# Kernel tuning notes

Hardware: AMD Instinct MI355X
Metric: run time of the kernel (lower is better)

The kernel has to match this reference:

```python
import jax, jax.numpy as jnp
import numpy as np

M, K, N = 8192, 4096, 4096

def setup_inputs() -> dict:
    key = jax.random.key(0)
    k1, k2 = jax.random.split(key)
    x_q = jax.random.randint(k1, (M, K), -128, 128, dtype=jnp.int8)
    weight_q = jax.random.randint(k2, (N, K), -128, 128, dtype=jnp.int8)
    scale_x = jnp.float32(0.02)
    weight_scale = jnp.float32(1.0)
    out_scale = jnp.float32(1.0)
    return {"x_q": x_q, "scale_x": scale_x, "weight_q": weight_q,
            "weight_scale": weight_scale, "out_scale": out_scale}

def reference(x_q, scale_x, weight_q, weight_scale, out_scale):
    # int8 GEMM with int32 accumulation: [M,K] @ [K,N] -> [M,N] int32
    acc = jnp.matmul(x_q.astype(jnp.int32), weight_q.T.astype(jnp.int32))
    # fused dequant + requant scale, then round/clamp back to int8
    scale = scale_x * weight_scale / out_scale
    y = acc.astype(jnp.float32) * scale
    y_q = jnp.clip(jnp.round(y), -128, 127).astype(jnp.int8)
    return (y_q, out_scale)
```

## Files before the change

kernel.cpp:

```cpp
#include <hip/hip_runtime.h>
#include <stdint.h>

#define M_DIM 8192
#define K_DIM 4096
#define N_DIM 4096
#define BM 128
#define BN 128
#define BK 64

typedef __attribute__((ext_vector_type(4))) int i32x4;

__global__ __launch_bounds__(256) void pack_kernel(const int* __restrict__ src,
                                                   int8_t* __restrict__ dst,
                                                   int n4) {
  const int stride = gridDim.x * 256;
  for (int i = blockIdx.x * 256 + threadIdx.x; i < n4; i += stride) {
    int4 v = reinterpret_cast<const int4*>(src)[i];
    int p = (v.x & 0xff) | ((v.y & 0xff) << 8) |
            ((v.z & 0xff) << 16) | ((v.w & 0xff) << 24);
    reinterpret_cast<int*>(dst)[i] = p;
  }
}

__global__ void tail_kernel(float* __restrict__ out, const float* __restrict__ so) {
  out[(size_t)M_DIM * N_DIM] = so[0];
}

template <bool DIRECT>
__global__ __launch_bounds__(256) void gemm_kernel(
    const int8_t* __restrict__ A8, const int8_t* __restrict__ B8,
    const int* __restrict__ A32, const int* __restrict__ B32,
    float* __restrict__ out,
    const float* __restrict__ sx, const float* __restrict__ sw,
    const float* __restrict__ so) {
  __shared__ int8_t As[BM * BK];
  __shared__ int8_t Bs[BN * BK];

  const int tid = threadIdx.x;
  const int lane = tid & 63;
  const int wid = tid >> 6;
  const int bid = blockIdx.x;
  const int bm = bid % (M_DIM / BM);
  const int bn = bid / (M_DIM / BM);
  const size_t arow0 = (size_t)bm * BM;
  const size_t bcol0 = (size_t)bn * BN;

  const int wrr = wid >> 1;
  const int wcc = wid & 1;
  const int lrow = lane & 15;
  const int kq = lane >> 4;

  i32x4 acc[4][4] = {};

  for (int kk = 0; kk < K_DIM; kk += BK) {
    if constexpr (!DIRECT) {
#pragma unroll
      for (int i = 0; i < 2; ++i) {
        int loff = i * 4096 + tid * 16;
        int r = loff >> 6, c = loff & 63;
        __builtin_amdgcn_global_load_lds(
            (const __attribute__((address_space(1))) void*)(A8 + (arow0 + r) * K_DIM + kk + c),
            (__attribute__((address_space(3))) void*)(As + loff), 16, 0, 0);
        __builtin_amdgcn_global_load_lds(
            (const __attribute__((address_space(1))) void*)(B8 + (bcol0 + r) * K_DIM + kk + c),
            (__attribute__((address_space(3))) void*)(Bs + loff), 16, 0, 0);
      }
    } else {
#pragma unroll
      for (int i = 0; i < 2; ++i) {
        int loff = i * 4096 + tid * 16;
        int r = loff >> 6, c = loff & 63;
        const int4* a4 = reinterpret_cast<const int4*>(A32 + (arow0 + r) * K_DIM + kk + c);
        const int4* b4 = reinterpret_cast<const int4*>(B32 + (bcol0 + r) * K_DIM + kk + c);
        int4 a0 = a4[0], a1 = a4[1], a2 = a4[2], a3 = a4[3];
        int4 b0 = b4[0], b1 = b4[1], b2 = b4[2], b3 = b4[3];
        int4 pa, pb;
        pa.x = (a0.x & 0xff) | ((a0.y & 0xff) << 8) | ((a0.z & 0xff) << 16) | ((a0.w & 0xff) << 24);
        pa.y = (a1.x & 0xff) | ((a1.y & 0xff) << 8) | ((a1.z & 0xff) << 16) | ((a1.w & 0xff) << 24);
        pa.z = (a2.x & 0xff) | ((a2.y & 0xff) << 8) | ((a2.z & 0xff) << 16) | ((a2.w & 0xff) << 24);
        pa.w = (a3.x & 0xff) | ((a3.y & 0xff) << 8) | ((a3.z & 0xff) << 16) | ((a3.w & 0xff) << 24);
        pb.x = (b0.x & 0xff) | ((b0.y & 0xff) << 8) | ((b0.z & 0xff) << 16) | ((b0.w & 0xff) << 24);
        pb.y = (b1.x & 0xff) | ((b1.y & 0xff) << 8) | ((b1.z & 0xff) << 16) | ((b1.w & 0xff) << 24);
        pb.z = (b2.x & 0xff) | ((b2.y & 0xff) << 8) | ((b2.z & 0xff) << 16) | ((b2.w & 0xff) << 24);
        pb.w = (b3.x & 0xff) | ((b3.y & 0xff) << 8) | ((b3.z & 0xff) << 16) | ((b3.w & 0xff) << 24);
        *reinterpret_cast<int4*>(As + loff) = pa;
        *reinterpret_cast<int4*>(Bs + loff) = pb;
      }
    }
    __syncthreads();

    i32x4 af[4], bf[4];
#pragma unroll
    for (int m = 0; m < 4; ++m)
      af[m] = *reinterpret_cast<const i32x4*>(As + (wrr * 64 + m * 16 + lrow) * BK + kq * 16);
#pragma unroll
    for (int n = 0; n < 4; ++n)
      bf[n] = *reinterpret_cast<const i32x4*>(Bs + (wcc * 64 + n * 16 + lrow) * BK + kq * 16);
#pragma unroll
    for (int m = 0; m < 4; ++m)
#pragma unroll
      for (int n = 0; n < 4; ++n)
        acc[m][n] = __builtin_amdgcn_mfma_i32_16x16x64_i8(af[m], bf[n], acc[m][n], 0, 0, 0);

    __syncthreads();
  }

  const float scale = sx[0] * sw[0] / so[0];
#pragma unroll
  for (int m = 0; m < 4; ++m) {
#pragma unroll
    for (int n = 0; n < 4; ++n) {
#pragma unroll
      for (int j = 0; j < 4; ++j) {
        int gr = (int)arow0 + wrr * 64 + m * 16 + kq * 4 + j;
        int gc = (int)bcol0 + wcc * 64 + n * 16 + lrow;
        float v = rintf((float)acc[m][n][j] * scale);
        v = fminf(fmaxf(v, -128.f), 127.f);
        out[(size_t)gr * N_DIM + gc] = v;
      }
    }
  }
}

extern "C" void kernel_launch(void* const* d_in, const int* in_sizes, int n_in,
                              void* d_out, int out_size, void* d_ws, size_t ws_size,
                              hipStream_t stream) {
  const int* x32 = (const int*)d_in[0];
  const float* sx = (const float*)d_in[1];
  const int* w32 = (const int*)d_in[2];
  const float* sw = (const float*)d_in[3];
  const float* so = (const float*)d_in[4];
  float* out = (float*)d_out;

  tail_kernel<<<1, 1, 0, stream>>>(out, so);

  const size_t a_bytes = (size_t)M_DIM * K_DIM;
  const size_t b_bytes = (size_t)N_DIM * K_DIM;
  const int grid = (M_DIM / BM) * (N_DIM / BN);

  if (ws_size >= a_bytes + b_bytes) {
    int8_t* A8 = (int8_t*)d_ws;
    int8_t* B8 = A8 + a_bytes;
    pack_kernel<<<2048, 256, 0, stream>>>(x32, A8, (int)(a_bytes / 4));
    pack_kernel<<<2048, 256, 0, stream>>>(w32, B8, (int)(b_bytes / 4));
    gemm_kernel<false><<<grid, 256, 0, stream>>>(A8, B8, nullptr, nullptr, out, sx, sw, so);
  } else {
    gemm_kernel<true><<<grid, 256, 0, stream>>>(nullptr, nullptr, x32, w32, out, sx, sw, so);
  }
}
```

Before: 437.7 us.

## Replace int8 GEMM with 256x256 double-buffered swizzled LDS kernel

Replaces the 128x128x64 single-buffered GEMM with a 512-thread kernel using 256x256x128 tiles, double-buffered LDS loads via global_load_lds, and an XOR swizzle to avoid bank conflicts. Block IDs are remapped to group tiles for L2 locality, and MFMA sections run at raised wave priority. This targets barrier stalls, exposed global load latency and reloading the same tiles from memory. In exchange it uses 128KB of LDS per block and many accumulator registers, which limits occupancy.

```diff
diff --git a/kernel.cpp b/kernel.cpp
--- a/kernel.cpp
+++ b/kernel.cpp
@@ -4,9 +4,6 @@
 #define M_DIM 8192
 #define K_DIM 4096
 #define N_DIM 4096
-#define BM 128
-#define BN 128
-#define BK 64
 
 typedef __attribute__((ext_vector_type(4))) int i32x4;
 
@@ -26,16 +23,132 @@
   out[(size_t)M_DIM * N_DIM] = so[0];
 }
 
-template <bool DIRECT>
-__global__ __launch_bounds__(256) void gemm_kernel(
+#define BM2 256
+#define BN2 256
+#define BK2 128
+#define NT  (K_DIM / BK2)
+
+#define ASM_VMCNT0 asm volatile("s_waitcnt vmcnt(0)" ::: "memory")
+#define ASM_LGKM0  asm volatile("s_waitcnt lgkmcnt(0)" ::: "memory")
+#define BARRIER()  asm volatile("s_barrier" ::: "memory")
+#define SCHEDB()   __builtin_amdgcn_sched_barrier(0)
+
+#define STAGE(KT, BUF) do { \
+  _Pragma("unroll") \
+  for (int c_ = 0; c_ < 4; ++c_) { \
+    const int8_t* ga_ = A8 + (size_t)(arow0 + c_*64 + srow) * K_DIM + (size_t)(KT)*BK2 + scol; \
+    __builtin_amdgcn_global_load_lds((const __attribute__((address_space(1))) void*)ga_, \
+        (__attribute__((address_space(3))) void*)(lds + (BUF)*65536 + c_*8192 + tid*16), 16, 0, 0); \
+  } \
+  _Pragma("unroll") \
+  for (int c_ = 0; c_ < 4; ++c_) { \
+    const int8_t* gb_ = B8 + (size_t)(bcol0 + c_*64 + srow) * K_DIM + (size_t)(KT)*BK2 + scol; \
+    __builtin_amdgcn_global_load_lds((const __attribute__((address_space(1))) void*)gb_, \
+        (__attribute__((address_space(3))) void*)(lds + (BUF)*65536 + 32768 + c_*8192 + tid*16), 16, 0, 0); \
+  } } while (0)
+
+__global__ __launch_bounds__(512, 2) void gemm2p(
     const int8_t* __restrict__ A8, const int8_t* __restrict__ B8,
+    float* __restrict__ out,
+    const float* __restrict__ sx, const float* __restrict__ sw,
+    const float* __restrict__ so) {
+  __shared__ __align__(16) int8_t lds[131072];
+
+  const int tid = threadIdx.x;
+  const int lane = tid & 63;
+  const int wid = tid >> 6;
+  const int wr = wid >> 2;
+  const int wc = wid & 3;
+  const int lrow = lane & 15;
+  const int kq = lane >> 4;
+
+  const int bid = blockIdx.x;
+  const int wg = (bid & 7) * 64 + (bid >> 3);
+  const int bm = wg & 31;
+  const int bn = wg >> 5;
+  const size_t arow0 = (size_t)bm * BM2;
+  const size_t bcol0 = (size_t)bn * BN2;
+
+  const int srow = tid >> 3;
+  const int scol = (((tid & 7) ^ ((tid >> 3) & 7)) << 4);
+
+  const int swz = (lrow & 7) << 4;
+  const int pc0 = (0  + kq * 16) ^ swz;
+  const int pc1 = (64 + kq * 16) ^ swz;
+  const int aoff = (wr * 128 + lrow) * 128;
+  const int boff = 32768 + (wc * 64 + lrow) * 128;
+
+  i32x4 acc[8][4] = {};
+  i32x4 af[8], bf[4];
+
+  STAGE(0, 0);
+  ASM_VMCNT0; BARRIER(); SCHEDB();
+
+  for (int kt = 0; kt < NT; ++kt) {
+    const int cb = kt & 1;
+    const int8_t* abase = lds + cb * 65536 + aoff;
+    const int8_t* bbase = lds + cb * 65536 + boff;
+    if (kt < NT - 1) STAGE(kt + 1, cb ^ 1);
+
+#pragma unroll
+    for (int m = 0; m < 8; ++m) af[m] = *(const i32x4*)(abase + m * 2048 + pc0);
+#pragma unroll
+    for (int n = 0; n < 4; ++n) bf[n] = *(const i32x4*)(bbase + n * 2048 + pc0);
+    ASM_LGKM0; SCHEDB();
+    __builtin_amdgcn_s_setprio(1);
+#pragma unroll
+    for (int m = 0; m < 8; ++m)
+#pragma unroll
+      for (int n = 0; n < 4; ++n)
+        acc[m][n] = __builtin_amdgcn_mfma_i32_16x16x64_i8(af[m], bf[n], acc[m][n], 0, 0, 0);
+    __builtin_amdgcn_s_setprio(0);
+
+#pragma unroll
+    for (int m = 0; m < 8; ++m) af[m] = *(const i32x4*)(abase + m * 2048 + pc1);
+#pragma unroll
+    for (int n = 0; n < 4; ++n) bf[n] = *(const i32x4*)(bbase + n * 2048 + pc1);
+    ASM_LGKM0; SCHEDB();
+    __builtin_amdgcn_s_setprio(1);
+#pragma unroll
+    for (int m = 0; m < 8; ++m)
+#pragma unroll
+      for (int n = 0; n < 4; ++n)
+        acc[m][n] = __builtin_amdgcn_mfma_i32_16x16x64_i8(af[m], bf[n], acc[m][n], 0, 0, 0);
+    __builtin_amdgcn_s_setprio(0);
+
+    ASM_VMCNT0; BARRIER(); SCHEDB();
+  }
+
+  const float s0 = *(volatile const float*)sx;
+  const float s1 = *(volatile const float*)sw;
+  const float s2 = *(volatile const float*)so;
+  const float scale = s0 * s1 / s2;
+#pragma unroll
+  for (int m = 0; m < 8; ++m) {
+#pragma unroll
+    for (int n = 0; n < 4; ++n) {
+#pragma unroll
+      for (int j = 0; j < 4; ++j) {
+        int gr = (int)arow0 + wr * 128 + m * 16 + kq * 4 + j;
+        int gc = (int)bcol0 + wc * 64 + n * 16 + lrow;
+        float v = rintf((float)acc[m][n][j] * scale);
+        v = fminf(fmaxf(v, -128.f), 127.f);
+        out[(size_t)gr * N_DIM + gc] = v;
+      }
+    }
+  }
+}
+
+#define BM 128
+#define BN 128
+#define BK 64
+__global__ __launch_bounds__(256) void gemm_direct(
     const int* __restrict__ A32, const int* __restrict__ B32,
     float* __restrict__ out,
     const float* __restrict__ sx, const float* __restrict__ sw,
     const float* __restrict__ so) {
   __shared__ int8_t As[BM * BK];
   __shared__ int8_t Bs[BN * BK];
-
   const int tid = threadIdx.x;
   const int lane = tid & 63;
   const int wid = tid >> 6;
@@ -44,72 +157,50 @@
   const int bn = bid / (M_DIM / BM);
   const size_t arow0 = (size_t)bm * BM;
   const size_t bcol0 = (size_t)bn * BN;
-
-  const int wrr = wid >> 1;
-  const int wcc = wid & 1;
-  const int lrow = lane & 15;
-  const int kq = lane >> 4;
-
+  const int wrr = wid >> 1, wcc = wid & 1;
+  const int lrow = lane & 15, kq = lane >> 4;
   i32x4 acc[4][4] = {};
-
   for (int kk = 0; kk < K_DIM; kk += BK) {
-    if constexpr (!DIRECT) {
-#pragma unroll
-      for (int i = 0; i < 2; ++i) {
-        int loff = i * 4096 + tid * 16;
-        int r = loff >> 6, c = loff & 63;
-        __builtin_amdgcn_global_load_lds(
-            (const __attribute__((address_space(1))) void*)(A8 + (arow0 + r) * K_DIM + kk + c),
-            (__attribute__((address_space(3))) void*)(As + loff), 16, 0, 0);
-        __builtin_amdgcn_global_load_lds(
-            (const __attribute__((address_space(1))) void*)(B8 + (bcol0 + r) * K_DIM + kk + c),
-            (__attribute__((address_space(3))) void*)(Bs + loff), 16, 0, 0);
-      }
-    } else {
-#pragma unroll
-      for (int i = 0; i < 2; ++i) {
-        int loff = i * 4096 + tid * 16;
-        int r = loff >> 6, c = loff & 63;
-        const int4* a4 = reinterpret_cast<const int4*>(A32 + (arow0 + r) * K_DIM + kk + c);
-        const int4* b4 = reinterpret_cast<const int4*>(B32 + (bcol0 + r) * K_DIM + kk + c);
-        int4 a0 = a4[0], a1 = a4[1], a2 = a4[2], a3 = a4[3];
-        int4 b0 = b4[0], b1 = b4[1], b2 = b4[2], b3 = b4[3];
-        int4 pa, pb;
-        pa.x = (a0.x & 0xff) | ((a0.y & 0xff) << 8) | ((a0.z & 0xff) << 16) | ((a0.w & 0xff) << 24);
-        pa.y = (a1.x & 0xff) | ((a1.y & 0xff) << 8) | ((a1.z & 0xff) << 16) | ((a1.w & 0xff) << 24);
-        pa.z = (a2.x & 0xff) | ((a2.y & 0xff) << 8) | ((a2.z & 0xff) << 16) | ((a2.w & 0xff) << 24);
-        pa.w = (a3.x & 0xff) | ((a3.y & 0xff) << 8) | ((a3.z & 0xff) << 16) | ((a3.w & 0xff) << 24);
-        pb.x = (b0.x & 0xff) | ((b0.y & 0xff) << 8) | ((b0.z & 0xff) << 16) | ((b0.w & 0xff) << 24);
-        pb.y = (b1.x & 0xff) | ((b1.y & 0xff) << 8) | ((b1.z & 0xff) << 16) | ((b1.w & 0xff) << 24);
-        pb.z = (b2.x & 0xff) | ((b2.y & 0xff) << 8) | ((b2.z & 0xff) << 16) | ((b2.w & 0xff) << 24);
-        pb.w = (b3.x & 0xff) | ((b3.y & 0xff) << 8) | ((b3.z & 0xff) << 16) | ((b3.w & 0xff) << 24);
-        *reinterpret_cast<int4*>(As + loff) = pa;
-        *reinterpret_cast<int4*>(Bs + loff) = pb;
-      }
+#pragma unroll
+    for (int i = 0; i < 2; ++i) {
+      int loff = i * 4096 + tid * 16;
+      int r = loff >> 6, c = loff & 63;
+      const int4* a4 = reinterpret_cast<const int4*>(A32 + (arow0 + r) * K_DIM + kk + c);
+      const int4* b4 = reinterpret_cast<const int4*>(B32 + (bcol0 + r) * K_DIM + kk + c);
+      int4 pa, pb;
+      int4 t0 = a4[0], t1 = a4[1], t2 = a4[2], t3 = a4[3];
+      pa.x = (t0.x & 0xff) | ((t0.y & 0xff) << 8) | ((t0.z & 0xff) << 16) | ((t0.w & 0xff) << 24);
+      pa.y = (t1.x & 0xff) | ((t1.y & 0xff) << 8) | ((t1.z & 0xff) << 16) | ((t1.w & 0xff) << 24);
+      pa.z = (t2.x & 0xff) | ((t2.y & 0xff) << 8) | ((t2.z & 0xff) << 16) | ((t2.w & 0xff) << 24);
+      pa.w = (t3.x & 0xff) | ((t3.y & 0xff) << 8) | ((t3.z & 0xff) << 16) | ((t3.w & 0xff) << 24);
+      t0 = b4[0]; t1 = b4[1]; t2 = b4[2]; t3 = b4[3];
+      pb.x = (t0.x & 0xff) | ((t0.y & 0xff) << 8) | ((t0.z & 0xff) << 16) | ((t0.w & 0xff) << 24);
+      pb.y = (t1.x & 0xff) | ((t1.y & 0xff) << 8) | ((t1.z & 0xff) << 16) | ((t1.w & 0xff) << 24);
+      pb.z = (t2.x & 0xff) | ((t2.y & 0xff) << 8) | ((t2.z & 0xff) << 16) | ((t2.w & 0xff) << 24);
+      pb.w = (t3.x & 0xff) | ((t3.y & 0xff) << 8) | ((t3.z & 0xff) << 16) | ((t3.w & 0xff) << 24);
+      *reinterpret_cast<int4*>(As + loff) = pa;
+      *reinterpret_cast<int4*>(Bs + loff) = pb;
     }
     __syncthreads();
-
-    i32x4 af[4], bf[4];
+    i32x4 afr[4], bfr[4];
 #pragma unroll
     for (int m = 0; m < 4; ++m)
-      af[m] = *reinterpret_cast<const i32x4*>(As + (wrr * 64 + m * 16 + lrow) * BK + kq * 16);
+      afr[m] = *reinterpret_cast<const i32x4*>(As + (wrr * 64 + m * 16 + lrow) * BK + kq * 16);
 #pragma unroll
     for (int n = 0; n < 4; ++n)
-      bf[n] = *reinterpret_cast<const i32x4*>(Bs + (wcc * 64 + n * 16 + lrow) * BK + kq * 16);
+      bfr[n] = *reinterpret_cast<const i32x4*>(Bs + (wcc * 64 + n * 16 + lrow) * BK + kq * 16);
 #pragma unroll
     for (int m = 0; m < 4; ++m)
 #pragma unroll
       for (int n = 0; n < 4; ++n)
-        acc[m][n] = __builtin_amdgcn_mfma_i32_16x16x64_i8(af[m], bf[n], acc[m][n], 0, 0, 0);
-
+        acc[m][n] = __builtin_amdgcn_mfma_i32_16x16x64_i8(afr[m], bfr[n], acc[m][n], 0, 0, 0);
     __syncthreads();
   }
-
   const float scale = sx[0] * sw[0] / so[0];
 #pragma unroll
-  for (int m = 0; m < 4; ++m) {
-#pragma unroll
-    for (int n = 0; n < 4; ++n) {
+  for (int m = 0; m < 4; ++m)
+#pragma unroll
+    for (int n = 0; n < 4; ++n)
 #pragma unroll
       for (int j = 0; j < 4; ++j) {
         int gr = (int)arow0 + wrr * 64 + m * 16 + kq * 4 + j;
@@ -118,8 +209,6 @@
         v = fminf(fmaxf(v, -128.f), 127.f);
         out[(size_t)gr * N_DIM + gc] = v;
       }
-    }
-  }
 }
 
 extern "C" void kernel_launch(void* const* d_in, const int* in_sizes, int n_in,
@@ -136,15 +225,16 @@
 
   const size_t a_bytes = (size_t)M_DIM * K_DIM;
   const size_t b_bytes = (size_t)N_DIM * K_DIM;
-  const int grid = (M_DIM / BM) * (N_DIM / BN);
 
   if (ws_size >= a_bytes + b_bytes) {
     int8_t* A8 = (int8_t*)d_ws;
     int8_t* B8 = A8 + a_bytes;
     pack_kernel<<<2048, 256, 0, stream>>>(x32, A8, (int)(a_bytes / 4));
     pack_kernel<<<2048, 256, 0, stream>>>(w32, B8, (int)(b_bytes / 4));
-    gemm_kernel<false><<<grid, 256, 0, stream>>>(A8, B8, nullptr, nullptr, out, sx, sw, so);
+    const int grid = (M_DIM / BM2) * (N_DIM / BN2);
+    gemm2p<<<grid, 512, 0, stream>>>(A8, B8, out, sx, sw, so);
   } else {
-    gemm_kernel<true><<<grid, 256, 0, stream>>>(nullptr, nullptr, x32, w32, out, sx, sw, so);
-  }
-}
+    const int grid = (M_DIM / BM) * (N_DIM / BN);
+    gemm_direct<<<grid, 256, 0, stream>>>(x32, w32, out, sx, sw, so);
+  }
+}
```

Measured after the change: 401.2 us. 1.09x faster.
